# Optimization experiments

Measured on AMD Instinct MI355X. Metric: run time of the kernel, lower is better.

The kernel has to match this reference:

```python
import jax, jax.numpy as jnp
import numpy as np

N = 100000   # nodes
DEG = 4      # fixed out-degree (>2 so every node survives the c>2 mask)
E = N * DEG  # edges
IN = 128
H = 256


def _lin_params(key, fan_out, fan_in, bias=True):
    k1, k2 = jax.random.split(key)
    W = 0.05 * jax.random.normal(k1, (fan_out, fan_in), jnp.float32)
    if bias:
        b = 0.05 * jax.random.normal(k2, (fan_out,), jnp.float32)
        return W, b
    return W


def setup_inputs() -> dict:
    key = jax.random.key(0)
    ks = jax.random.split(key, 12)
    x = jax.random.normal(ks[0], (N, IN), jnp.float32)
    # every node has exactly DEG outgoing edges -> out-degree 4 > 2 for all nodes
    src = jnp.repeat(jnp.arange(N, dtype=jnp.int32), DEG)
    dst = jax.random.randint(ks[1], (E,), 0, N, dtype=jnp.int32)
    edge_index = jnp.stack([src, dst])  # [2, E]
    batch = jnp.zeros((N,), jnp.int32)
    Wr0, br0 = _lin_params(ks[2], H, IN)
    Ws0 = _lin_params(ks[3], H, IN, bias=False)
    Wr1, br1 = _lin_params(ks[4], H, H)
    Ws1 = _lin_params(ks[5], H, H, bias=False)
    Wr2, br2 = _lin_params(ks[6], H, H)
    Ws2 = _lin_params(ks[7], H, H, bias=False)
    Wsp1, bsp1 = _lin_params(ks[8], 1, H)
    Wsp2, bsp2 = _lin_params(ks[9], 1, H)
    Wl, bl = _lin_params(ks[10], 1, 2)
    return dict(x=x, edge_index=edge_index, batch=batch,
                Wr0=Wr0, br0=br0, Ws0=Ws0,
                Wr1=Wr1, br1=br1, Ws1=Ws1,
                Wr2=Wr2, br2=br2, Ws2=Ws2,
                Wsp1=Wsp1, bsp1=bsp1, Wsp2=Wsp2, bsp2=bsp2,
                Wl=Wl, bl=bl)


def reference(x, edge_index, batch, Wr0, br0, Ws0, Wr1, br1, Ws1,
              Wr2, br2, Ws2, Wsp1, bsp1, Wsp2, bsp2, Wl, bl):
    src, dst = edge_index[0], edge_index[1]

    def gconv(h, Wr, br, Ws):
        # PyG GraphConv(aggr='add'): out_i = W_rel @ sum_{j->i} h_j + b + W_root @ h_i
        agg = jax.ops.segment_sum(h[src], dst, num_segments=N)
        return jax.nn.relu(agg @ Wr.T + br + h @ Ws.T)

    h = gconv(x, Wr0, br0, Ws0)
    h = gconv(h, Wr1, br1, Ws1)
    h = gconv(h, Wr2, br2, Ws2)

    # unique(edge_index[0], counts) ; keep source nodes with out-degree > 2
    deg = jax.ops.segment_sum(jnp.ones((E,), h.dtype), src, num_segments=N)
    sel = jnp.nonzero(deg > 2, size=N, fill_value=0)[0]  # all N nodes by construction
    xs = h[sel].reshape(-1, 2 * H)  # pair consecutive nodes
    x1, x2 = xs[:, :H], xs[:, H:]
    out = jnp.concatenate([jax.nn.relu(x1 @ Wsp1.T + bsp1),
                           jax.nn.relu(x2 @ Wsp2.T + bsp2)], axis=1)
    y = jax.nn.sigmoid(out @ Wl.T + bl)  # split=True branch
    return y, xs, x1, x2
```

## Files before the change

kernel.cpp:

```cpp
#include <hip/hip_runtime.h>
#include <hip/hip_bf16.h>
#include <math.h>

#define NNODES 100000
#define NEDGES 400000
#define INDIM  128
#define HDIM   256
#define MAXDEG 32

#define BM 64
#define BN 256
#define MTILES 1563

typedef __attribute__((ext_vector_type(8))) short short8;
typedef __attribute__((ext_vector_type(8))) unsigned short ushort8v;
typedef __attribute__((ext_vector_type(4))) float f32x4;

__device__ __forceinline__ float bf2f(unsigned short u) {
    union { unsigned int i; float f; } v; v.i = ((unsigned int)u) << 16; return v.f;
}
__device__ __forceinline__ unsigned short f2bf(float f) {
    union { float f; unsigned int i; } v; v.f = f;
    unsigned int r = v.i + 0x7fffu + ((v.i >> 16) & 1u);
    return (unsigned short)(r >> 16);
}

__device__ __forceinline__ void async_load16(const void* g, void* l) {
    __builtin_amdgcn_global_load_lds(
        (const __attribute__((address_space(1))) unsigned int*)g,
        (__attribute__((address_space(3))) unsigned int*)l,
        16, 0, 0);
}

#define XB_BLOCKS 12500
#define W0_BLOCKS 256
#define W1_BLOCKS 512
#define EL_BLOCKS 1563
#define PREP_BLOCKS (XB_BLOCKS + W0_BLOCKS + 2 * W1_BLOCKS + EL_BLOCKS)

__global__ void prep_kernel(const float* __restrict__ x, unsigned short* __restrict__ xb,
                            const float* __restrict__ Wr0, const float* __restrict__ Ws0,
                            unsigned short* __restrict__ B0,
                            const float* __restrict__ Wr1, const float* __restrict__ Ws1,
                            unsigned short* __restrict__ B1,
                            const float* __restrict__ Wr2, const float* __restrict__ Ws2,
                            unsigned short* __restrict__ B2,
                            const int* __restrict__ ei, int* __restrict__ cnt,
                            int* __restrict__ elist) {
    int b = blockIdx.x;
    if (b < XB_BLOCKS) {
        int i = b * 256 + threadIdx.x;
        float4 v = ((const float4*)x)[i];
        ushort4 o; o.x = f2bf(v.x); o.y = f2bf(v.y); o.z = f2bf(v.z); o.w = f2bf(v.w);
        ((ushort4*)xb)[i] = o;
        return;
    }
    b -= XB_BLOCKS;
    if (b < W0_BLOCKS + 2 * W1_BLOCKS) {
        const float *Wr, *Ws; unsigned short* B; int K;
        if (b < W0_BLOCKS)               { Wr = Wr0; Ws = Ws0; B = B0; K = INDIM; }
        else if (b < W0_BLOCKS + W1_BLOCKS) { Wr = Wr1; Ws = Ws1; B = B1; K = HDIM; b -= W0_BLOCKS; }
        else                              { Wr = Wr2; Ws = Ws2; B = B2; K = HDIM; b -= W0_BLOCKS + W1_BLOCKS; }
        int idx = b * 256 + threadIdx.x;
        int n = idx / (2 * K);
        int k = idx - n * 2 * K;
        float v = (k < K) ? Wr[n * K + k] : Ws[n * K + (k - K)];
        B[idx] = f2bf(v);
        return;
    }
    b -= W0_BLOCKS + 2 * W1_BLOCKS;
    int e = b * 256 + threadIdx.x;
    if (e < NEDGES) {
        int d = ei[NEDGES + e];
        int s = ei[e];
        int pos = atomicAdd(&cnt[d], 1);
        if (pos < MAXDEG) elist[d * MAXDEG + pos] = s;
    }
}

template<int MODE, int K>
__global__ __launch_bounds__(256, 2)
void fused_gconv(const unsigned short* __restrict__ h,
                 const int* __restrict__ cnt, const int* __restrict__ elist,
                 const unsigned short* __restrict__ B, const float* __restrict__ bias,
                 unsigned short* __restrict__ hout,
                 float* __restrict__ xs, float* __restrict__ x1o, float* __restrict__ x2o,
                 const float* __restrict__ Wsp1, const float* __restrict__ Wsp2,
                 float* __restrict__ spart) {
    __shared__ __align__(16) unsigned char smem[64 * K * 2 * 2];
    unsigned short* Agg  = (unsigned short*)smem;
    unsigned short* A2sh = (unsigned short*)(smem + 64 * K * 2);

    const int tid  = threadIdx.x;
    const int lane = tid & 63;
    const int wv   = tid >> 6;
    const int m0   = blockIdx.x * BM;
    constexpr int Ktot = 2 * K;
    constexpr int SEGS = K / 8;

    const int lane31 = lane & 31;
    const int hw     = lane >> 5;
    int pn = m0 + wv * 16 + (lane >> 2);
    if (pn >= NNODES) pn = NNODES - 1;
    const int4 elv = ((const int4*)(elist + (size_t)pn * MAXDEG))[lane & 3];
    int cnode = m0 + wv * 16 + (lane & 15);
    if (cnode >= NNODES) cnode = NNODES - 1;
    const int cv = cnt[cnode];

    #pragma unroll
    for (int it = 0; it < (64 * SEGS) / 256; it++) {
        int idx = it * 256 + tid;
        int row = idx / SEGS, seg = idx % SEGS;
        int gseg = (seg & ~7) | ((seg ^ (row & 7)) & 7);
        int grow = m0 + row; if (grow >= NNODES) grow = NNODES - 1;
        async_load16(h + (size_t)grow * K + gseg * 8, &A2sh[idx * 8]);
    }

    if constexpr (K == 256) {
        for (int rd = 0; rd < 8; rd++) {
            const int iw = rd * 2 + hw;
            int cA = __shfl(cv, rd * 2);
            int cB = __shfl(cv, rd * 2 + 1);
            if (cA > MAXDEG) cA = MAXDEG;
            if (cB > MAXDEG) cB = MAXDEG;
            const int c    = hw ? cB : cA;
            const int cmax = cA > cB ? cA : cB;
            int node = m0 + wv * 16 + iw;
            if (node >= NNODES) node = NNODES - 1;
            float a[8];
            #pragma unroll
            for (int i = 0; i < 8; i++) a[i] = 0.f;
            for (int j0 = 0; j0 < cmax; j0 += 4) {
                int4 e;
                if (j0 < 16) {
                    int src = iw * 4 + (j0 >> 2);
                    e.x = __shfl(elv.x, src); e.y = __shfl(elv.y, src);
                    e.z = __shfl(elv.z, src); e.w = __shfl(elv.w, src);
                } else {
                    e = ((const int4*)(elist + (size_t)node * MAXDEG))[j0 >> 2];
                }
                int rem = c - j0;
                ushort8v v0 = {0,0,0,0,0,0,0,0}, v1 = v0, v2 = v0, v3 = v0;
                if (rem > 0) v0 = ((const ushort8v*)(h + (size_t)e.x * 256))[lane31];
                if (rem > 1) v1 = ((const ushort8v*)(h + (size_t)e.y * 256))[lane31];
                if (rem > 2) v2 = ((const ushort8v*)(h + (size_t)e.z * 256))[lane31];
                if (rem > 3) v3 = ((const ushort8v*)(h + (size_t)e.w * 256))[lane31];
                #pragma unroll
                for (int i = 0; i < 8; i++)
                    a[i] += bf2f(v0[i]) + bf2f(v1[i]) + bf2f(v2[i]) + bf2f(v3[i]);
            }
            int r = wv * 16 + iw;
            int sgp = (lane31 & ~7) | ((lane31 ^ r) & 7);
            ushort8v o;
            #pragma unroll
            for (int i = 0; i < 8; i++) o[i] = f2bf(a[i]);
            *(ushort8v*)&Agg[r * 256 + sgp * 8] = o;
        }
    } else {
        for (int rd = 0; rd < 8; rd++) {
            const int iw = rd * 2 + hw;
            int cA = __shfl(cv, rd * 2);
            int cB = __shfl(cv, rd * 2 + 1);
            if (cA > MAXDEG) cA = MAXDEG;
            if (cB > MAXDEG) cB = MAXDEG;
            const int c    = hw ? cB : cA;
            const int cmax = cA > cB ? cA : cB;
            int node = m0 + wv * 16 + iw;
            if (node >= NNODES) node = NNODES - 1;
            float a0 = 0.f, a1 = 0.f, a2 = 0.f, a3 = 0.f;
            for (int j0 = 0; j0 < cmax; j0 += 4) {
                int4 e;
                if (j0 < 16) {
                    int src = iw * 4 + (j0 >> 2);
                    e.x = __shfl(elv.x, src); e.y = __shfl(elv.y, src);
                    e.z = __shfl(elv.z, src); e.w = __shfl(elv.w, src);
                } else {
                    e = ((const int4*)(elist + (size_t)node * MAXDEG))[j0 >> 2];
                }
                int rem = c - j0;
                ushort4 v0 = {0,0,0,0}, v1 = {0,0,0,0}, v2 = {0,0,0,0}, v3 = {0,0,0,0};
                if (rem > 0) v0 = ((const ushort4*)(h + (size_t)e.x * 128))[lane31];
                if (rem > 1) v1 = ((const ushort4*)(h + (size_t)e.y * 128))[lane31];
                if (rem > 2) v2 = ((const ushort4*)(h + (size_t)e.z * 128))[lane31];
                if (rem > 3) v3 = ((const ushort4*)(h + (size_t)e.w * 128))[lane31];
                a0 += bf2f(v0.x) + bf2f(v1.x) + bf2f(v2.x) + bf2f(v3.x);
                a1 += bf2f(v0.y) + bf2f(v1.y) + bf2f(v2.y) + bf2f(v3.y);
                a2 += bf2f(v0.z) + bf2f(v1.z) + bf2f(v2.z) + bf2f(v3.z);
                a3 += bf2f(v0.w) + bf2f(v1.w) + bf2f(v2.w) + bf2f(v3.w);
            }
            int r = wv * 16 + iw;
            int sg = lane31 >> 1;
            int sgp = (sg & ~7) | ((sg ^ r) & 7);
            ushort4 o; o.x = f2bf(a0); o.y = f2bf(a1); o.z = f2bf(a2); o.w = f2bf(a3);
            *(ushort4*)&Agg[r * 128 + sgp * 8 + (lane31 & 1) * 4] = o;
        }
    }

    __syncthreads();

    f32x4 acc[4][4];
    #pragma unroll
    for (int i = 0; i < 4; i++)
        #pragma unroll
        for (int j = 0; j < 4; j++)
            acc[i][j] = (f32x4){0.f, 0.f, 0.f, 0.f};

    const int l15  = lane & 15;
    const int seg0 = lane >> 4;

    #pragma unroll
    for (int k0 = 0; k0 < K; k0 += 64) {
        #pragma unroll
        for (int half = 0; half < 2; half++) {
            const int sg = (k0 >> 3) + half * 4 + seg0;
            short8 afr[4], afs[4], bwr[4], bws[4];
            #pragma unroll
            for (int nt = 0; nt < 4; nt++) {
                int nl = wv * 64 + nt * 16 + l15;
                bwr[nt] = *(const short8*)(B + (size_t)nl * Ktot + sg * 8);
                bws[nt] = *(const short8*)(B + (size_t)nl * Ktot + K + sg * 8);
            }
            #pragma unroll
            for (int mt = 0; mt < 4; mt++) {
                int ml  = mt * 16 + l15;
                int sgp = (sg & ~7) | ((sg ^ ml) & 7);
                afr[mt] = *(const short8*)&Agg [ml * K + sgp * 8];
                afs[mt] = *(const short8*)&A2sh[ml * K + sgp * 8];
            }
            #pragma unroll
            for (int mt = 0; mt < 4; mt++)
                #pragma unroll
                for (int nt = 0; nt < 4; nt++)
                    acc[mt][nt] = __builtin_amdgcn_mfma_f32_16x16x32_bf16(
                        afr[mt], bwr[nt], acc[mt][nt], 0, 0, 0);
            #pragma unroll
            for (int mt = 0; mt < 4; mt++)
                #pragma unroll
                for (int nt = 0; nt < 4; nt++)
                    acc[mt][nt] = __builtin_amdgcn_mfma_f32_16x16x32_bf16(
                        afs[mt], bws[nt], acc[mt][nt], 0, 0, 0);
        }
    }

    float* bounce = (float*)smem;
    float* wb = bounce + wv * (16 * 68);
    const int q    = lane & 3;
    const int rrow = lane >> 2;

    #pragma unroll
    for (int mt = 0; mt < 4; mt++) {
        __syncthreads();
        #pragma unroll
        for (int nt = 0; nt < 4; nt++)
            #pragma unroll
            for (int rr = 0; rr < 4; rr++)
                wb[((lane >> 4) * 4 + rr) * 68 + nt * 16 + (lane & 15)] = acc[mt][nt][rr];
        __syncthreads();

        int grow = m0 + mt * 16 + rrow;
        int gc   = wv * 64 + q * 16;
        float4 v[4];
        #pragma unroll
        for (int s = 0; s < 4; s++)
            v[s] = ((const float4*)(wb + rrow * 68 + q * 16))[s];

        if (grow < NNODES) {
            const float4* bv = (const float4*)(bias + gc);
            #pragma unroll
            for (int s = 0; s < 4; s++) {
                float4 b4 = bv[s];
                v[s].x = fmaxf(v[s].x + b4.x, 0.f);
                v[s].y = fmaxf(v[s].y + b4.y, 0.f);
                v[s].z = fmaxf(v[s].z + b4.z, 0.f);
                v[s].w = fmaxf(v[s].w + b4.w, 0.f);
            }
            if (MODE == 0) {
                ushort8v o0, o1;
                o0[0]=f2bf(v[0].x); o0[1]=f2bf(v[0].y); o0[2]=f2bf(v[0].z); o0[3]=f2bf(v[0].w);
                o0[4]=f2bf(v[1].x); o0[5]=f2bf(v[1].y); o0[6]=f2bf(v[1].z); o0[7]=f2bf(v[1].w);
                o1[0]=f2bf(v[2].x); o1[1]=f2bf(v[2].y); o1[2]=f2bf(v[2].z); o1[3]=f2bf(v[2].w);
                o1[4]=f2bf(v[3].x); o1[5]=f2bf(v[3].y); o1[6]=f2bf(v[3].z); o1[7]=f2bf(v[3].w);
                ushort8v* dst = (ushort8v*)(hout + (size_t)grow * HDIM + gc);
                dst[0] = o0; dst[1] = o1;
            } else {
                float4* xsp = (float4*)(xs + (size_t)grow * HDIM + gc);
                #pragma unroll
                for (int s = 0; s < 4; s++) xsp[s] = v[s];
                float* xo = (grow & 1) ? x2o : x1o;
                float4* xop = (float4*)(xo + (size_t)(grow >> 1) * HDIM + gc);
                #pragma unroll
                for (int s = 0; s < 4; s++) xop[s] = v[s];
                const float* wsp = (grow & 1) ? Wsp2 : Wsp1;
                const float4* wv4 = (const float4*)(wsp + gc);
                float p = 0.f;
                #pragma unroll
                for (int s = 0; s < 4; s++) {
                    float4 w4 = wv4[s];
                    p += v[s].x * w4.x + v[s].y * w4.y + v[s].z * w4.z + v[s].w * w4.w;
                }
                p += __shfl_xor(p, 1);
                p += __shfl_xor(p, 2);
                if (q == 0) atomicAdd(&spart[grow], p);
            }
        }
    }
}

__global__ void finalize_kernel(const float* __restrict__ spart, const float* __restrict__ bsp1,
                                const float* __restrict__ bsp2, const float* __restrict__ Wl,
                                const float* __restrict__ bl, float* __restrict__ y) {
    int p = blockIdx.x * 256 + threadIdx.x;
    if (p < NNODES / 2) {
        float s1 = spart[2 * p]     + bsp1[0]; s1 = s1 > 0.f ? s1 : 0.f;
        float s2 = spart[2 * p + 1] + bsp2[0]; s2 = s2 > 0.f ? s2 : 0.f;
        float t = s1 * Wl[0] + s2 * Wl[1] + bl[0];
        y[p] = 1.f / (1.f + expf(-t));
    }
}

extern "C" void kernel_launch(void* const* d_in, const int* in_sizes, int n_in,
                              void* d_out, int out_size, void* d_ws, size_t ws_size,
                              hipStream_t stream) {
    const float* x    = (const float*)d_in[0];
    const int*   ei   = (const int*)d_in[1];
    const float* Wr0  = (const float*)d_in[3];
    const float* br0  = (const float*)d_in[4];
    const float* Ws0  = (const float*)d_in[5];
    const float* Wr1  = (const float*)d_in[6];
    const float* br1  = (const float*)d_in[7];
    const float* Ws1  = (const float*)d_in[8];
    const float* Wr2  = (const float*)d_in[9];
    const float* br2  = (const float*)d_in[10];
    const float* Ws2  = (const float*)d_in[11];
    const float* Wsp1 = (const float*)d_in[12];
    const float* bsp1 = (const float*)d_in[13];
    const float* Wsp2 = (const float*)d_in[14];
    const float* bsp2 = (const float*)d_in[15];
    const float* Wl   = (const float*)d_in[16];
    const float* bl   = (const float*)d_in[17];

    char* ws = (char*)d_ws;
    size_t off = 0;
    auto alloc = [&](size_t bytes) -> void* {
        void* p = ws + off;
        off += (bytes + 255) & ~(size_t)255;
        return p;
    };
    int*            cnt   = (int*)alloc((size_t)NNODES * 4);
    float*          spart = (float*)alloc((size_t)NNODES * 4);
    size_t zero_bytes = off;
    int*            elist = (int*)alloc((size_t)NNODES * MAXDEG * 4);
    unsigned short* xb    = (unsigned short*)alloc((size_t)NNODES * INDIM * 2);
    unsigned short* hA    = (unsigned short*)alloc((size_t)NNODES * HDIM * 2);
    unsigned short* hB    = (unsigned short*)alloc((size_t)NNODES * HDIM * 2);
    unsigned short* B0    = (unsigned short*)alloc((size_t)HDIM * 2 * INDIM * 2);
    unsigned short* B1    = (unsigned short*)alloc((size_t)HDIM * 2 * HDIM * 2);
    unsigned short* B2    = (unsigned short*)alloc((size_t)HDIM * 2 * HDIM * 2);

    float* y  = (float*)d_out;
    float* xs = y + 50000;
    float* x1 = xs + (size_t)50000 * 512;
    float* x2 = x1 + (size_t)50000 * 256;

    hipMemsetAsync(ws, 0, zero_bytes, stream);
    prep_kernel<<<PREP_BLOCKS, 256, 0, stream>>>(x, xb, Wr0, Ws0, B0, Wr1, Ws1, B1,
                                                 Wr2, Ws2, B2, ei, cnt, elist);

    fused_gconv<0, 128><<<MTILES, 256, 0, stream>>>(xb, cnt, elist, B0, br0, hA,
                                                    nullptr, nullptr, nullptr,
                                                    nullptr, nullptr, nullptr);
    fused_gconv<0, 256><<<MTILES, 256, 0, stream>>>(hA, cnt, elist, B1, br1, hB,
                                                    nullptr, nullptr, nullptr,
                                                    nullptr, nullptr, nullptr);
    fused_gconv<1, 256><<<MTILES, 256, 0, stream>>>(hB, cnt, elist, B2, br2, nullptr,
                                                    xs, x1, x2, Wsp1, Wsp2, spart);
    finalize_kernel<<<(NNODES / 2 + 255) / 256, 256, 0, stream>>>(
        spart, bsp1, bsp2, Wl, bl, y);
}
```

Measured before the change: 625.9 us.

## Use 512-thread blocks with 8 waves splitting nodes and output columns

Each fused GraphConv block now runs 8 waves instead of 4. Each wave gathers 8 nodes instead of 16 and computes a 32-column slice of the GEMM instead of 64. The edge list preload is widened so all 32 neighbor slots come from registers via shuffles, with no global refetch. The first 8 neighbors are issued as one unrolled batch of loads to raise memory-level parallelism. This halves per-wave accumulators and raises occupancy, at the cost of more B-fragment reloads per block and extra barrier participants.

```diff
diff --git a/kernel.cpp b/kernel.cpp
--- a/kernel.cpp
+++ b/kernel.cpp
@@ -30,6 +30,13 @@
         (const __attribute__((address_space(1))) unsigned int*)g,
         (__attribute__((address_space(3))) unsigned int*)l,
         16, 0, 0);
+}
+
+__device__ __forceinline__ int4 shfl4(const int4 v, int src) {
+    int4 r;
+    r.x = __shfl(v.x, src); r.y = __shfl(v.y, src);
+    r.z = __shfl(v.z, src); r.w = __shfl(v.w, src);
+    return r;
 }
 
 #define XB_BLOCKS 12500
@@ -79,7 +86,7 @@
 }
 
 template<int MODE, int K>
-__global__ __launch_bounds__(256, 2)
+__global__ __launch_bounds__(512, 4)
 void fused_gconv(const unsigned short* __restrict__ h,
                  const int* __restrict__ cnt, const int* __restrict__ elist,
                  const unsigned short* __restrict__ B, const float* __restrict__ bias,
@@ -100,95 +107,112 @@
 
     const int lane31 = lane & 31;
     const int hw     = lane >> 5;
-    int pn = m0 + wv * 16 + (lane >> 2);
+    int pn = m0 + wv * 8 + (lane >> 3);
     if (pn >= NNODES) pn = NNODES - 1;
-    const int4 elv = ((const int4*)(elist + (size_t)pn * MAXDEG))[lane & 3];
-    int cnode = m0 + wv * 16 + (lane & 15);
+    const int4 elv = ((const int4*)(elist + (size_t)pn * MAXDEG))[lane & 7];
+    int cnode = m0 + wv * 8 + (lane & 7);
     if (cnode >= NNODES) cnode = NNODES - 1;
     const int cv = cnt[cnode];
 
     #pragma unroll
-    for (int it = 0; it < (64 * SEGS) / 256; it++) {
-        int idx = it * 256 + tid;
+    for (int it = 0; it < (64 * SEGS) / 512; it++) {
+        int idx = it * 512 + tid;
         int row = idx / SEGS, seg = idx % SEGS;
         int gseg = (seg & ~7) | ((seg ^ (row & 7)) & 7);
         int grow = m0 + row; if (grow >= NNODES) grow = NNODES - 1;
         async_load16(h + (size_t)grow * K + gseg * 8, &A2sh[idx * 8]);
     }
 
-    if constexpr (K == 256) {
-        for (int rd = 0; rd < 8; rd++) {
-            const int iw = rd * 2 + hw;
-            int cA = __shfl(cv, rd * 2);
-            int cB = __shfl(cv, rd * 2 + 1);
-            if (cA > MAXDEG) cA = MAXDEG;
-            if (cB > MAXDEG) cB = MAXDEG;
-            const int c    = hw ? cB : cA;
-            const int cmax = cA > cB ? cA : cB;
-            int node = m0 + wv * 16 + iw;
-            if (node >= NNODES) node = NNODES - 1;
+    #pragma unroll
+    for (int rd = 0; rd < 4; rd++) {
+        const int iw = rd * 2 + hw;
+        int cA = __shfl(cv, rd * 2);
+        int cB = __shfl(cv, rd * 2 + 1);
+        if (cA > MAXDEG) cA = MAXDEG;
+        if (cB > MAXDEG) cB = MAXDEG;
+        const int c    = hw ? cB : cA;
+        const int cmax = cA > cB ? cA : cB;
+        const int4 e0 = shfl4(elv, iw * 8 + 0);
+        const int4 e1 = shfl4(elv, iw * 8 + 1);
+
+        if constexpr (K == 256) {
             float a[8];
             #pragma unroll
             for (int i = 0; i < 8; i++) a[i] = 0.f;
-            for (int j0 = 0; j0 < cmax; j0 += 4) {
-                int4 e;
-                if (j0 < 16) {
-                    int src = iw * 4 + (j0 >> 2);
-                    e.x = __shfl(elv.x, src); e.y = __shfl(elv.y, src);
-                    e.z = __shfl(elv.z, src); e.w = __shfl(elv.w, src);
-                } else {
-                    e = ((const int4*)(elist + (size_t)node * MAXDEG))[j0 >> 2];
-                }
+            ushort8v z = {0,0,0,0,0,0,0,0};
+            ushort8v v0 = z, v1 = z, v2 = z, v3 = z;
+            ushort8v w0 = z, w1 = z, w2 = z, w3 = z;
+            if (c > 0) v0 = ((const ushort8v*)(h + (size_t)e0.x * 256))[lane31];
+            if (c > 1) v1 = ((const ushort8v*)(h + (size_t)e0.y * 256))[lane31];
+            if (c > 2) v2 = ((const ushort8v*)(h + (size_t)e0.z * 256))[lane31];
+            if (c > 3) v3 = ((const ushort8v*)(h + (size_t)e0.w * 256))[lane31];
+            if (cmax > 4) {
+                int r2 = c - 4;
+                if (r2 > 0) w0 = ((const ushort8v*)(h + (size_t)e1.x * 256))[lane31];
+                if (r2 > 1) w1 = ((const ushort8v*)(h + (size_t)e1.y * 256))[lane31];
+                if (r2 > 2) w2 = ((const ushort8v*)(h + (size_t)e1.z * 256))[lane31];
+                if (r2 > 3) w3 = ((const ushort8v*)(h + (size_t)e1.w * 256))[lane31];
+            }
+            #pragma unroll
+            for (int i = 0; i < 8; i++)
+                a[i] += (bf2f(v0[i]) + bf2f(v1[i]) + bf2f(v2[i]) + bf2f(v3[i]))
+                      + (bf2f(w0[i]) + bf2f(w1[i]) + bf2f(w2[i]) + bf2f(w3[i]));
+            for (int j0 = 8; j0 < cmax; j0 += 4) {
+                int4 e = shfl4(elv, iw * 8 + (j0 >> 2));
                 int rem = c - j0;
-                ushort8v v0 = {0,0,0,0,0,0,0,0}, v1 = v0, v2 = v0, v3 = v0;
-                if (rem > 0) v0 = ((const ushort8v*)(h + (size_t)e.x * 256))[lane31];
-                if (rem > 1) v1 = ((const ushort8v*)(h + (size_t)e.y * 256))[lane31];
-                if (rem > 2) v2 = ((const ushort8v*)(h + (size_t)e.z * 256))[lane31];
-                if (rem > 3) v3 = ((const ushort8v*)(h + (size_t)e.w * 256))[lane31];
+                ushort8v t0 = z, t1 = z, t2 = z, t3 = z;
+                if (rem > 0) t0 = ((const ushort8v*)(h + (size_t)e.x * 256))[lane31];
+                if (rem > 1) t1 = ((const ushort8v*)(h + (size_t)e.y * 256))[lane31];
+                if (rem > 2) t2 = ((const ushort8v*)(h + (size_t)e.z * 256))[lane31];
+                if (rem > 3) t3 = ((const ushort8v*)(h + (size_t)e.w * 256))[lane31];
                 #pragma unroll
                 for (int i = 0; i < 8; i++)
-                    a[i] += bf2f(v0[i]) + bf2f(v1[i]) + bf2f(v2[i]) + bf2f(v3[i]);
-            }
-            int r = wv * 16 + iw;
+                    a[i] += bf2f(t0[i]) + bf2f(t1[i]) + bf2f(t2[i]) + bf2f(t3[i]);
+            }
+            int r = wv * 8 + iw;
             int sgp = (lane31 & ~7) | ((lane31 ^ r) & 7);
             ushort8v o;
             #pragma unroll
             for (int i = 0; i < 8; i++) o[i] = f2bf(a[i]);
             *(ushort8v*)&Agg[r * 256 + sgp * 8] = o;
-        }
-    } else {
-        for (int rd = 0; rd < 8; rd++) {
-            const int iw = rd * 2 + hw;
-            int cA = __shfl(cv, rd * 2);
-            int cB = __shfl(cv, rd * 2 + 1);
-            if (cA > MAXDEG) cA = MAXDEG;
-            if (cB > MAXDEG) cB = MAXDEG;
-            const int c    = hw ? cB : cA;
-            const int cmax = cA > cB ? cA : cB;
-            int node = m0 + wv * 16 + iw;
-            if (node >= NNODES) node = NNODES - 1;
+        } else {
             float a0 = 0.f, a1 = 0.f, a2 = 0.f, a3 = 0.f;
-            for (int j0 = 0; j0 < cmax; j0 += 4) {
-                int4 e;
-                if (j0 < 16) {
-                    int src = iw * 4 + (j0 >> 2);
-                    e.x = __shfl(elv.x, src); e.y = __shfl(elv.y, src);
-                    e.z = __shfl(elv.z, src); e.w = __shfl(elv.w, src);
-                } else {
-                    e = ((const int4*)(elist + (size_t)node * MAXDEG))[j0 >> 2];
-                }
+            ushort4 z = {0,0,0,0};
+            ushort4 v0 = z, v1 = z, v2 = z, v3 = z;
+            ushort4 w0 = z, w1 = z, w2 = z, w3 = z;
+            if (c > 0) v0 = ((const ushort4*)(h + (size_t)e0.x * 128))[lane31];
+            if (c > 1) v1 = ((const ushort4*)(h + (size_t)e0.y * 128))[lane31];
+            if (c > 2) v2 = ((const ushort4*)(h + (size_t)e0.z * 128))[lane31];
+            if (c > 3) v3 = ((const ushort4*)(h + (size_t)e0.w * 128))[lane31];
+            if (cmax > 4) {
+                int r2 = c - 4;
+                if (r2 > 0) w0 = ((const ushort4*)(h + (size_t)e1.x * 128))[lane31];
+                if (r2 > 1) w1 = ((const ushort4*)(h + (size_t)e1.y * 128))[lane31];
+                if (r2 > 2) w2 = ((const ushort4*)(h + (size_t)e1.z * 128))[lane31];
+                if (r2 > 3) w3 = ((const ushort4*)(h + (size_t)e1.w * 128))[lane31];
+            }
+            a0 += bf2f(v0.x) + bf2f(v1.x) + bf2f(v2.x) + bf2f(v3.x)
+                + bf2f(w0.x) + bf2f(w1.x) + bf2f(w2.x) + bf2f(w3.x);
+            a1 += bf2f(v0.y) + bf2f(v1.y) + bf2f(v2.y) + bf2f(v3.y)
+                + bf2f(w0.y) + bf2f(w1.y) + bf2f(w2.y) + bf2f(w3.y);
+            a2 += bf2f(v0.z) + bf2f(v1.z) + bf2f(v2.z) + bf2f(v3.z)
+                + bf2f(w0.z) + bf2f(w1.z) + bf2f(w2.z) + bf2f(w3.z);
+            a3 += bf2f(v0.w) + bf2f(v1.w) + bf2f(v2.w) + bf2f(v3.w)
+                + bf2f(w0.w) + bf2f(w1.w) + bf2f(w2.w) + bf2f(w3.w);
+            for (int j0 = 8; j0 < cmax; j0 += 4) {
+                int4 e = shfl4(elv, iw * 8 + (j0 >> 2));
                 int rem = c - j0;
-                ushort4 v0 = {0,0,0,0}, v1 = {0,0,0,0}, v2 = {0,0,0,0}, v3 = {0,0,0,0};
-                if (rem > 0) v0 = ((const ushort4*)(h + (size_t)e.x * 128))[lane31];
-                if (rem > 1) v1 = ((const ushort4*)(h + (size_t)e.y * 128))[lane31];
-                if (rem > 2) v2 = ((const ushort4*)(h + (size_t)e.z * 128))[lane31];
-                if (rem > 3) v3 = ((const ushort4*)(h + (size_t)e.w * 128))[lane31];
-                a0 += bf2f(v0.x) + bf2f(v1.x) + bf2f(v2.x) + bf2f(v3.x);
-                a1 += bf2f(v0.y) + bf2f(v1.y) + bf2f(v2.y) + bf2f(v3.y);
-                a2 += bf2f(v0.z) + bf2f(v1.z) + bf2f(v2.z) + bf2f(v3.z);
-                a3 += bf2f(v0.w) + bf2f(v1.w) + bf2f(v2.w) + bf2f(v3.w);
-            }
-            int r = wv * 16 + iw;
+                ushort4 t0 = z, t1 = z, t2 = z, t3 = z;
+                if (rem > 0) t0 = ((const ushort4*)(h + (size_t)e.x * 128))[lane31];
+                if (rem > 1) t1 = ((const ushort4*)(h + (size_t)e.y * 128))[lane31];
+                if (rem > 2) t2 = ((const ushort4*)(h + (size_t)e.z * 128))[lane31];
+                if (rem > 3) t3 = ((const ushort4*)(h + (size_t)e.w * 128))[lane31];
+                a0 += bf2f(t0.x) + bf2f(t1.x) + bf2f(t2.x) + bf2f(t3.x);
+                a1 += bf2f(t0.y) + bf2f(t1.y) + bf2f(t2.y) + bf2f(t3.y);
+                a2 += bf2f(t0.z) + bf2f(t1.z) + bf2f(t2.z) + bf2f(t3.z);
+                a3 += bf2f(t0.w) + bf2f(t1.w) + bf2f(t2.w) + bf2f(t3.w);
+            }
+            int r = wv * 8 + iw;
             int sg = lane31 >> 1;
             int sgp = (sg & ~7) | ((sg ^ r) & 7);
             ushort4 o; o.x = f2bf(a0); o.y = f2bf(a1); o.z = f2bf(a2); o.w = f2bf(a3);
@@ -198,11 +222,11 @@
 
     __syncthreads();
 
-    f32x4 acc[4][4];
+    f32x4 acc[4][2];
     #pragma unroll
     for (int i = 0; i < 4; i++)
         #pragma unroll
-        for (int j = 0; j < 4; j++)
+        for (int j = 0; j < 2; j++)
             acc[i][j] = (f32x4){0.f, 0.f, 0.f, 0.f};
 
     const int l15  = lane & 15;
@@ -213,10 +237,10 @@
         #pragma unroll
         for (int half = 0; half < 2; half++) {
             const int sg = (k0 >> 3) + half * 4 + seg0;
-            short8 afr[4], afs[4], bwr[4], bws[4];
-            #pragma unroll
-            for (int nt = 0; nt < 4; nt++) {
-                int nl = wv * 64 + nt * 16 + l15;
+            short8 afr[4], afs[4], bwr[2], bws[2];
+            #pragma unroll
+            for (int nt = 0; nt < 2; nt++) {
+                int nl = wv * 32 + nt * 16 + l15;
                 bwr[nt] = *(const short8*)(B + (size_t)nl * Ktot + sg * 8);
                 bws[nt] = *(const short8*)(B + (size_t)nl * Ktot + K + sg * 8);
             }
@@ -230,20 +254,20 @@
             #pragma unroll
             for (int mt = 0; mt < 4; mt++)
                 #pragma unroll
-                for (int nt = 0; nt < 4; nt++)
+                for (int nt = 0; nt < 2; nt++)
                     acc[mt][nt] = __builtin_amdgcn_mfma_f32_16x16x32_bf16(
                         afr[mt], bwr[nt], acc[mt][nt], 0, 0, 0);
             #pragma unroll
             for (int mt = 0; mt < 4; mt++)
                 #pragma unroll
-                for (int nt = 0; nt < 4; nt++)
+                for (int nt = 0; nt < 2; nt++)
                     acc[mt][nt] = __builtin_amdgcn_mfma_f32_16x16x32_bf16(
                         afs[mt], bws[nt], acc[mt][nt], 0, 0, 0);
         }
     }
 
     float* bounce = (float*)smem;
-    float* wb = bounce + wv * (16 * 68);
+    float* wb = bounce + wv * (16 * 40);
     const int q    = lane & 3;
     const int rrow = lane >> 2;
 
@@ -251,53 +275,42 @@
     for (int mt = 0; mt < 4; mt++) {
         __syncthreads();
         #pragma unroll
-        for (int nt = 0; nt < 4; nt++)
+        for (int nt = 0; nt < 2; nt++)
             #pragma unroll
             for (int rr = 0; rr < 4; rr++)
-                wb[((lane >> 4) * 4 + rr) * 68 + nt * 16 + (lane & 15)] = acc[mt][nt][rr];
+                wb[((lane >> 4) * 4 + rr) * 40 + nt * 16 + l15] = acc[mt][nt][rr];
         __syncthreads();
 
         int grow = m0 + mt * 16 + rrow;
-        int gc   = wv * 64 + q * 16;
-        float4 v[4];
-        #pragma unroll
-        for (int s = 0; s < 4; s++)
-            v[s] = ((const float4*)(wb + rrow * 68 + q * 16))[s];
+        int gc0  = wv * 32 + q * 4;
+        int gc1  = gc0 + 16;
+        float4 v0 = *(const float4*)(wb + rrow * 40 + q * 4);
+        float4 v1 = *(const float4*)(wb + rrow * 40 + 16 + q * 4);
 
         if (grow < NNODES) {
-            const float4* bv = (const float4*)(bias + gc);
-            #pragma unroll
-            for (int s = 0; s < 4; s++) {
-                float4 b4 = bv[s];
-                v[s].x = fmaxf(v[s].x + b4.x, 0.f);
-                v[s].y = fmaxf(v[s].y + b4.y, 0.f);
-                v[s].z = fmaxf(v[s].z + b4.z, 0.f);
-                v[s].w = fmaxf(v[s].w + b4.w, 0.f);
-            }
+            float4 b0 = *(const float4*)(bias + gc0);
+            float4 b1 = *(const float4*)(bias + gc1);
+            v0.x = fmaxf(v0.x + b0.x, 0.f); v0.y = fmaxf(v0.y + b0.y, 0.f);
+            v0.z = fmaxf(v0.z + b0.z, 0.f); v0.w = fmaxf(v0.w + b0.w, 0.f);
+            v1.x = fmaxf(v1.x + b1.x, 0.f); v1.y = fmaxf(v1.y + b1.y, 0.f);
+            v1.z = fmaxf(v1.z + b1.z, 0.f); v1.w = fmaxf(v1.w + b1.w, 0.f);
             if (MODE == 0) {
-                ushort8v o0, o1;
-                o0[0]=f2bf(v[0].x); o0[1]=f2bf(v[0].y); o0[2]=f2bf(v[0].z); o0[3]=f2bf(v[0].w);
-                o0[4]=f2bf(v[1].x); o0[5]=f2bf(v[1].y); o0[6]=f2bf(v[1].z); o0[7]=f2bf(v[1].w);
-                o1[0]=f2bf(v[2].x); o1[1]=f2bf(v[2].y); o1[2]=f2bf(v[2].z); o1[3]=f2bf(v[2].w);
-                o1[4]=f2bf(v[3].x); o1[5]=f2bf(v[3].y); o1[6]=f2bf(v[3].z); o1[7]=f2bf(v[3].w);
-                ushort8v* dst = (ushort8v*)(hout + (size_t)grow * HDIM + gc);
-                dst[0] = o0; dst[1] = o1;
+                ushort4 o0, o1;
+                o0.x = f2bf(v0.x); o0.y = f2bf(v0.y); o0.z = f2bf(v0.z); o0.w = f2bf(v0.w);
+                o1.x = f2bf(v1.x); o1.y = f2bf(v1.y); o1.z = f2bf(v1.z); o1.w = f2bf(v1.w);
+                *(ushort4*)(hout + (size_t)grow * HDIM + gc0) = o0;
+                *(ushort4*)(hout + (size_t)grow * HDIM + gc1) = o1;
             } else {
-                float4* xsp = (float4*)(xs + (size_t)grow * HDIM + gc);
-                #pragma unroll
-                for (int s = 0; s < 4; s++) xsp[s] = v[s];
+                *(float4*)(xs + (size_t)grow * HDIM + gc0) = v0;
+                *(float4*)(xs + (size_t)grow * HDIM + gc1) = v1;
                 float* xo = (grow & 1) ? x2o : x1o;
-                float4* xop = (float4*)(xo + (size_t)(grow >> 1) * HDIM + gc);
-                #pragma unroll
-                for (int s = 0; s < 4; s++) xop[s] = v[s];
+                *(float4*)(xo + (size_t)(grow >> 1) * HDIM + gc0) = v0;
+                *(float4*)(xo + (size_t)(grow >> 1) * HDIM + gc1) = v1;
                 const float* wsp = (grow & 1) ? Wsp2 : Wsp1;
-                const float4* wv4 = (const float4*)(wsp + gc);
-                float p = 0.f;
-                #pragma unroll
-                for (int s = 0; s < 4; s++) {
-                    float4 w4 = wv4[s];
-                    p += v[s].x * w4.x + v[s].y * w4.y + v[s].z * w4.z + v[s].w * w4.w;
-                }
+                float4 w0 = *(const float4*)(wsp + gc0);
+                float4 w1 = *(const float4*)(wsp + gc1);
+                float p = v0.x * w0.x + v0.y * w0.y + v0.z * w0.z + v0.w * w0.w
+                        + v1.x * w1.x + v1.y * w1.y + v1.z * w1.z + v1.w * w1.w;
                 p += __shfl_xor(p, 1);
                 p += __shfl_xor(p, 2);
                 if (q == 0) atomicAdd(&spart[grow], p);
@@ -366,13 +379,13 @@
     prep_kernel<<<PREP_BLOCKS, 256, 0, stream>>>(x, xb, Wr0, Ws0, B0, Wr1, Ws1, B1,
                                                  Wr2, Ws2, B2, ei, cnt, elist);
 
-    fused_gconv<0, 128><<<MTILES, 256, 0, stream>>>(xb, cnt, elist, B0, br0, hA,
+    fused_gconv<0, 128><<<MTILES, 512, 0, stream>>>(xb, cnt, elist, B0, br0, hA,
                                                     nullptr, nullptr, nullptr,
                                                     nullptr, nullptr, nullptr);
-    fused_gconv<0, 256><<<MTILES, 256, 0, stream>>>(hA, cnt, elist, B1, br1, hB,
+    fused_gconv<0, 256><<<MTILES, 512, 0, stream>>>(hA, cnt, elist, B1, br1, hB,
                                                     nullptr, nullptr, nullptr,
                                                     nullptr, nullptr, nullptr);
-    fused_gconv<1, 256><<<MTILES, 256, 0, stream>>>(hB, cnt, elist, B2, br2, nullptr,
+    fused_gconv<1, 256><<<MTILES, 512, 0, stream>>>(hB, cnt, elist, B2, br2, nullptr,
                                                     xs, x1, x2, Wsp1, Wsp2, spart);
     finalize_kernel<<<(NNODES / 2 + 255) / 256, 256, 0, stream>>>(
         spart, bsp1, bsp2, Wl, bl, y);
```

After: 554.6 us. 1.13x faster.
